# Kernel optimization log

Hardware: AMD Instinct MI355X
Metric: run time of the kernel (lower is better)

## Reference

```python
import jax, jax.numpy as jnp
import numpy as np

B, N, DIM = 4, 2048, 1024
HEADS, DHEAD = 16, 64
INNER = HEADS * DHEAD  # 1024


def _sigma(t):
    # elu(x) + 1 feature map (strictly positive)
    return jax.nn.elu(t) + 1.0


def setup_inputs() -> dict:
    key = jax.random.key(0)
    k1, k2, k3, k4, k5 = jax.random.split(key, 5)
    x = jax.random.normal(k1, (B, N, DIM), dtype=jnp.float32)
    M = jax.random.normal(k2, (B, HEADS, DHEAD, DHEAD), dtype=jnp.float32)
    Z = jnp.ones((B, HEADS, DHEAD, 1), dtype=jnp.float32)
    W_qkv = jax.random.normal(k3, (DIM, 3 * INNER), dtype=jnp.float32) * (DIM ** -0.5)
    beta_lin = jnp.ones((1,), dtype=jnp.float32) * 4.6     # Linear_Attention.beta
    beta_gate = jax.random.normal(k4, (1, HEADS, 1, 1), dtype=jnp.float32)  # per-head gate
    return {"x": x, "M": M, "Z": Z, "W_qkv": W_qkv, "beta_lin": beta_lin, "beta_gate": beta_gate}


def reference(x, M, Z, W_qkv, beta_lin, beta_gate):
    b, n, _ = x.shape
    scale = DHEAD ** -0.5

    qkv = x @ W_qkv                                   # [b, n, 3*inner]
    q, k, v = jnp.split(qkv, 3, axis=-1)
    # b n (h d) -> b h n d
    to_heads = lambda t: t.reshape(b, n, HEADS, DHEAD).transpose(0, 2, 1, 3)
    q, k, v = to_heads(q), to_heads(k), to_heads(v)

    # ---- linear-attention compressive memory branch ----
    sq = _sigma(q)                                    # [b h n d]
    sk = _sigma(k)
    A_mem = jnp.einsum('bhnd,bhdv->bhnv', sq, M) / jnp.einsum('bhnd,bhdi->bhni', sq, Z)
    moment = jnp.einsum('bhnd,bhdv->bhnv', sk, M) / jnp.einsum('bhnd,bhdi->bhni', sk, Z)

    # EMA state update (training path)
    beta_m = jnp.clip(jax.nn.sigmoid(beta_lin), 0.9, 0.999)  # scalar in (0.9, 0.999)
    Z_new = beta_m * Z + jnp.sum(sk, axis=-2)[..., None]      # [b h d 1]
    M_new = beta_m * M + jnp.einsum('bhnd,bhnv->bhdv', sk, v - moment)

    # ---- standard dot-product attention branch ----
    dots = jnp.einsum('bhid,bhjd->bhij', q, k) * scale
    attn = jax.nn.softmax(dots, axis=-1)
    A_dot = jnp.einsum('bhij,bhjd->bhid', attn, v)

    # ---- learned per-head gate ----
    g = jax.nn.sigmoid(beta_gate)                     # [1 h 1 1]
    A = g * A_mem + (1.0 - g) * A_dot                 # [b h n d]
    A = A.transpose(0, 2, 1, 3).reshape(b, n, INNER)  # b h n d -> b n (h d)
    return (A, M_new, Z_new)
```

## Files before the change

kernel.cpp:

```cpp
#include <hip/hip_runtime.h>
#include <math.h>

#define B_ 4
#define N_ 2048
#define DIM_ 1024
#define H_ 16
#define D_ 64
#define INNER_ 1024
#define BH_ (B_*H_)

#define A_ELEMS  (B_*N_*INNER_)
#define M_ELEMS  (BH_*D_*D_)
#define Z_ELEMS  (BH_*D_)

#define SC_LOG2E 0.18033688011112042f

typedef __attribute__((ext_vector_type(8))) short short8;
typedef __attribute__((ext_vector_type(4))) float f32x4;
typedef __attribute__((ext_vector_type(4))) unsigned short us4;
typedef unsigned short u16;

typedef const unsigned int __attribute__((address_space(1))) gu32;
typedef unsigned int __attribute__((address_space(3))) su32;

__device__ __forceinline__ u16 f2bf(float f) {
    unsigned int u = __float_as_uint(f);
    u += 0x7fffu + ((u >> 16) & 1u);
    return (u16)(u >> 16);
}
__device__ __forceinline__ float bf2f(u16 s) {
    return __uint_as_float(((unsigned int)s) << 16);
}
__device__ __forceinline__ float sigma_f(float x) {
    return x > 0.f ? x + 1.f : __expf(x);
}
__device__ __forceinline__ short8 sig8(short8 in) {
    short8 out;
    u16* ip = (u16*)&in; u16* op = (u16*)&out;
    #pragma unroll
    for (int c = 0; c < 8; c++) op[c] = f2bf(sigma_f(bf2f(ip[c])));
    return out;
}

__global__ __launch_bounds__(256) void cvt_x(const float* __restrict__ x,
                                             u16* __restrict__ xb) {
    long i = ((long)blockIdx.x * 256 + threadIdx.x) * 4;
    float4 f = *(const float4*)&x[i];
    us4 o = {f2bf(f.x), f2bf(f.y), f2bf(f.z), f2bf(f.w)};
    *(us4*)&xb[i] = o;
}

__global__ __launch_bounds__(256) void cvt_w(const float* __restrict__ W,
                                             u16* __restrict__ Wt) {
    __shared__ u16 T[64 * 68];
    const int t  = threadIdx.x;
    const int n0 = blockIdx.x * 64, k0 = blockIdx.y * 64;
    #pragma unroll
    for (int i = 0; i < 4; i++) {
        int r  = (t >> 4) + i * 16;
        int c4 = (t & 15) * 4;
        float4 f = *(const float4*)&W[(long)(k0 + r) * 3072 + n0 + c4];
        T[(c4 + 0) * 68 + r] = f2bf(f.x);
        T[(c4 + 1) * 68 + r] = f2bf(f.y);
        T[(c4 + 2) * 68 + r] = f2bf(f.z);
        T[(c4 + 3) * 68 + r] = f2bf(f.w);
    }
    __syncthreads();
    #pragma unroll
    for (int i = 0; i < 4; i++) {
        int n  = (t >> 4) + i * 16;
        int k4 = (t & 15) * 4;
        us4 o;
        o.x = T[n * 68 + k4];     o.y = T[n * 68 + k4 + 1];
        o.z = T[n * 68 + k4 + 2]; o.w = T[n * 68 + k4 + 3];
        *(us4*)&Wt[(long)(n0 + n) * 1024 + k0 + k4] = o;
    }
}

__global__ __launch_bounds__(256) void qkv_mfma(
    const u16* __restrict__ xb, const u16* __restrict__ Wt,
    u16* __restrict__ q, u16* __restrict__ k, u16* __restrict__ v,
    u16* __restrict__ qs) {
    __shared__ u16 As[128 * 64];
    __shared__ u16 Bs[128 * 64];
    const int t = threadIdx.x, w = t >> 6, lane = t & 63;
    const int quad = lane >> 4, l16 = lane & 15;
    const int m0 = blockIdx.y * 128, j0 = blockIdx.x * 128;
    const int mw = (w >> 1) * 64, nw = (w & 1) * 64;

    const int row0 = t >> 3;
    const int cg   = (t & 7) * 8;

    f32x4 acc[4][4] = {};

    for (int k0 = 0; k0 < DIM_; k0 += 64) {
        __syncthreads();
        #pragma unroll
        for (int i = 0; i < 4; i++) {
            int r = row0 + i * 32;
            __builtin_amdgcn_global_load_lds(
                (gu32*)&xb[(long)(m0 + r) * 1024 + k0 + cg],
                (su32*)&As[r * 64 + cg], 16, 0, 0);
            __builtin_amdgcn_global_load_lds(
                (gu32*)&Wt[(long)(j0 + r) * 1024 + k0 + cg],
                (su32*)&Bs[r * 64 + cg], 16, 0, 0);
        }
        __syncthreads();

        #pragma unroll
        for (int kk = 0; kk < 2; kk++) {
            short8 af[4], bf[4];
            #pragma unroll
            for (int mt = 0; mt < 4; mt++)
                af[mt] = *(const short8*)&As[(mw + mt * 16 + l16) * 64 + kk * 32 + quad * 8];
            #pragma unroll
            for (int nt = 0; nt < 4; nt++)
                bf[nt] = *(const short8*)&Bs[(nw + nt * 16 + l16) * 64 + kk * 32 + quad * 8];
            #pragma unroll
            for (int mt = 0; mt < 4; mt++)
                #pragma unroll
                for (int nt = 0; nt < 4; nt++)
                    acc[mt][nt] = __builtin_amdgcn_mfma_f32_16x16x32_bf16(
                        af[mt], bf[nt], acc[mt][nt], 0, 0, 0);
        }
    }

    #pragma unroll
    for (int mt = 0; mt < 4; mt++) {
        #pragma unroll
        for (int r = 0; r < 4; r++) {
            int mm = m0 + mw + mt * 16 + quad * 4 + r;
            int b  = mm >> 11, n = mm & 2047;
            #pragma unroll
            for (int nt = 0; nt < 4; nt++) {
                int col   = j0 + nw + nt * 16 + l16;
                int which = col >> 10;
                int rem   = col & 1023;
                int h = rem >> 6, d = rem & 63;
                long idx = (((long)(b * H_ + h)) * N_ + n) * D_ + d;
                float a = acc[mt][nt][r];
                u16 val = f2bf(a);
                if (which == 0) {
                    q[idx]  = val;
                    qs[idx] = f2bf(a * SC_LOG2E);
                } else {
                    u16* dst = (which == 1) ? k : v;
                    dst[idx] = val;
                }
            }
        }
    }
}

__global__ __launch_bounds__(256) void vt_transpose(
    const u16* __restrict__ vb, u16* __restrict__ vT) {
    __shared__ u16 T[64 * 72];
    const int bh = blockIdx.y;
    const int n0 = blockIdx.x * 64;
    const int t  = threadIdx.x;
    const int jj = t >> 3, kg = (t & 7) * 8;
    #pragma unroll
    for (int i = 0; i < 2; i++) {
        int j = jj + i * 32;
        short8 vv = *(const short8*)&vb[(((long)bh * N_ + n0 + j) << 6) + kg];
        u16* vp = (u16*)&vv;
        int jc = j ^ kg;
        #pragma unroll
        for (int c = 0; c < 8; c++) T[(kg + c) * 72 + jc] = vp[c];
    }
    __syncthreads();
    const int d = t >> 2, sg = (t & 3) * 16, xr = d & 56;
    short8 a0 = *(const short8*)&T[d * 72 + (sg ^ xr)];
    short8 a1 = *(const short8*)&T[d * 72 + ((sg + 8) ^ xr)];
    u16* dst = vT + ((long)bh * 64 + d) * 2048 + n0 + sg;
    *(short8*)dst       = a0;
    *(short8*)(dst + 8) = a1;
}

__global__ __launch_bounds__(256) void init_mz(
    const float* __restrict__ M, const float* __restrict__ Z,
    const float* __restrict__ beta_lin,
    float* __restrict__ outM, float* __restrict__ outZ) {
    float beta = 1.f / (1.f + __expf(-beta_lin[0]));
    beta = fminf(fmaxf(beta, 0.9f), 0.999f);
    int i = blockIdx.x * 256 + threadIdx.x;
    if (i < M_ELEMS) outM[i] = beta * M[i];
    if (i < Z_ELEMS) outZ[i] = beta * Z[i];
}

__global__ __launch_bounds__(256) void linear_mfma(
    const u16* __restrict__ qg, const u16* __restrict__ kg_,
    const u16* __restrict__ vTg, const float* __restrict__ Mg,
    const float* __restrict__ Zg, const float* __restrict__ beta_gate,
    float* __restrict__ outA, float* __restrict__ outM, float* __restrict__ outZ) {
    __shared__ u16 MTz[80 * 72];
    __shared__ u16 sqsh[64 * 72];
    __shared__ u16 sksh[64 * 72];
    __shared__ u16 skT[64 * 72];
    __shared__ u16 vT[64 * 72];
    __shared__ u16 vmT[80 * 72];
    __shared__ float dks[64];

    const int bh = blockIdx.y, b = bh >> 4, h = bh & 15;
    const int t = threadIdx.x, w = t >> 6, lane = t & 63;
    const int quad = lane >> 4, l16 = lane & 15;
    const long bhN = (long)bh * N_;

    #pragma unroll
    for (int i = 0; i < 4; i++) {
        int d  = (t >> 4) + i * 16;
        int c4 = (t & 15) * 4;
        float4 f = *(const float4*)&Mg[bh * 4096 + d * 64 + c4];
        MTz[(c4 + 0) * 72 + d] = f2bf(f.x);
        MTz[(c4 + 1) * 72 + d] = f2bf(f.y);
        MTz[(c4 + 2) * 72 + d] = f2bf(f.z);
        MTz[(c4 + 3) * 72 + d] = f2bf(f.w);
    }
    if (t < 64) {
        MTz[64 * 72 + t] = f2bf(Zg[bh * 64 + t]);
        vmT[64 * 72 + t] = f2bf(1.0f);
    }
    for (int e = t; e < 15 * 72; e += 256) {
        MTz[65 * 72 + e] = 0;
        vmT[65 * 72 + e] = 0;
    }
    if (t >= 64 && t < 72) { MTz[64 * 72 + t] = 0; vmT[64 * 72 + t] = 0; }

    const float g = 1.f / (1.f + __expf(-beta_gate[h]));

    f32x4 macc[5] = {};

    const int jj = t >> 3;
    const int kgp = (t & 7) * 8;
    const int srow = t >> 2;
    const int sg   = (t & 3) * 16;

    for (int c0 = 0; c0 < 256; c0 += 64) {
        const int n0c = blockIdx.x * 256 + c0;
        __syncthreads();

        #pragma unroll
        for (int i = 0; i < 2; i++) {
            int j = jj + i * 32;
            long gb = ((bhN + n0c + j) << 6) + kgp;
            short8 q8 = sig8(*(const short8*)&qg[gb]);
            short8 k8 = sig8(*(const short8*)&kg_[gb]);
            *(short8*)&sqsh[j * 72 + kgp] = q8;
            *(short8*)&sksh[j * 72 + kgp] = k8;
            u16* kp = (u16*)&k8;
            int jc = j ^ kgp;
            #pragma unroll
            for (int c = 0; c < 8; c++) skT[(kgp + c) * 72 + jc] = kp[c];
        }
        {
            const u16* vp = vTg + ((long)bh * 64 + srow) * 2048 + n0c + sg;
            *(short8*)&vT[srow * 72 + sg]     = *(const short8*)vp;
            *(short8*)&vT[srow * 72 + sg + 8] = *(const short8*)(vp + 8);
        }
        __syncthreads();

        {
            short8 a0 = *(const short8*)&sqsh[(w * 16 + l16) * 72 + quad * 8];
            short8 a1 = *(const short8*)&sqsh[(w * 16 + l16) * 72 + 32 + quad * 8];
            f32x4 am[5];
            #pragma unroll
            for (int ct = 0; ct < 5; ct++) {
                short8 b0 = *(const short8*)&MTz[(ct * 16 + l16) * 72 + quad * 8];
                short8 b1 = *(const short8*)&MTz[(ct * 16 + l16) * 72 + 32 + quad * 8];
                f32x4 acc = {};
                acc = __builtin_amdgcn_mfma_f32_16x16x32_bf16(a0, b0, acc, 0, 0, 0);
                acc = __builtin_amdgcn_mfma_f32_16x16x32_bf16(a1, b1, acc, 0, 0, 0);
                am[ct] = acc;
            }
            #pragma unroll
            for (int r = 0; r < 4; r++) {
                float dq  = __shfl(am[4][r], lane & 48, 64);
                float inv = __builtin_amdgcn_rcpf(dq);
                int n = n0c + w * 16 + quad * 4 + r;
                long row = ((long)(b * N_ + n)) * INNER_ + h * 64;
                #pragma unroll
                for (int ct = 0; ct < 4; ct++)
                    outA[row + ct * 16 + l16] = g * am[ct][r] * inv;
            }
        }

        f32x4 mt_[4];
        {
            short8 a0 = *(const short8*)&MTz[(w * 16 + l16) * 72 + quad * 8];
            short8 a1 = *(const short8*)&MTz[(w * 16 + l16) * 72 + 32 + quad * 8];
            #pragma unroll
            for (int ct = 0; ct < 4; ct++) {
                short8 b0 = *(const short8*)&sksh[(ct * 16 + l16) * 72 + quad * 8];
                short8 b1 = *(const short8*)&sksh[(ct * 16 + l16) * 72 + 32 + quad * 8];
                f32x4 acc = {};
                acc = __builtin_amdgcn_mfma_f32_16x16x32_bf16(a0, b0, acc, 0, 0, 0);
                acc = __builtin_amdgcn_mfma_f32_16x16x32_bf16(a1, b1, acc, 0, 0, 0);
                mt_[ct] = acc;
            }
            short8 z0 = *(const short8*)&MTz[(64 + l16) * 72 + quad * 8];
            short8 z1 = *(const short8*)&MTz[(64 + l16) * 72 + 32 + quad * 8];
            short8 b0 = *(const short8*)&sksh[(w * 16 + l16) * 72 + quad * 8];
            short8 b1 = *(const short8*)&sksh[(w * 16 + l16) * 72 + 32 + quad * 8];
            f32x4 acc = {};
            acc = __builtin_amdgcn_mfma_f32_16x16x32_bf16(z0, b0, acc, 0, 0, 0);
            acc = __builtin_amdgcn_mfma_f32_16x16x32_bf16(z1, b1, acc, 0, 0, 0);
            if (quad == 0) dks[w * 16 + l16] = __builtin_amdgcn_rcpf(acc[0]);
        }
        __syncthreads();

        #pragma unroll
        for (int ct = 0; ct < 4; ct++) {
            float invdk = dks[ct * 16 + l16];
            #pragma unroll
            for (int r = 0; r < 4; r++) {
                int vd = w * 16 + quad * 4 + r;
                float vv = bf2f(vT[vd * 72 + ct * 16 + l16]);
                vmT[vd * 72 + ct * 16 + l16] = f2bf(vv - mt_[ct][r] * invdk);
            }
        }
        __syncthreads();

        {
            int drow = w * 16 + l16, xr = drow & 56;
            short8 a0 = *(const short8*)&skT[drow * 72 + ((quad * 8) ^ xr)];
            short8 a1 = *(const short8*)&skT[drow * 72 + ((32 + quad * 8) ^ xr)];
            #pragma unroll
            for (int ct = 0; ct < 5; ct++) {
                short8 b0 = *(const short8*)&vmT[(ct * 16 + l16) * 72 + quad * 8];
                short8 b1 = *(const short8*)&vmT[(ct * 16 + l16) * 72 + 32 + quad * 8];
                macc[ct] = __builtin_amdgcn_mfma_f32_16x16x32_bf16(a0, b0, macc[ct], 0, 0, 0);
                macc[ct] = __builtin_amdgcn_mfma_f32_16x16x32_bf16(a1, b1, macc[ct], 0, 0, 0);
            }
        }
    }

    #pragma unroll
    for (int ct = 0; ct < 4; ct++)
        #pragma unroll
        for (int r = 0; r < 4; r++) {
            int d = w * 16 + quad * 4 + r;
            atomicAdd(&outM[bh * 4096 + d * 64 + ct * 16 + l16], macc[ct][r]);
        }
    if (l16 == 0)
        #pragma unroll
        for (int r = 0; r < 4; r++)
            atomicAdd(&outZ[bh * 64 + w * 16 + quad * 4 + r], macc[4][r]);
}

__global__ __launch_bounds__(256) void flash_mfma(
    const u16* __restrict__ qsb, const u16* __restrict__ kb,
    const u16* __restrict__ vTg, const float* __restrict__ beta_gate,
    float* __restrict__ outA) {
    __shared__ u16 Ks[64 * 72];
    __shared__ u16 Vt[64 * 72];

    const int bh = blockIdx.y, b = bh >> 4, h = bh & 15;
    const int n0 = blockIdx.x * 128;
    const int t = threadIdx.x, w = t >> 6, lane = t & 63;
    const int quad = lane >> 4, l16 = lane & 15;
    const long bhN = (long)bh * N_;

    const int srow = t >> 2;
    const int sg   = (t & 3) * 16;
    const int jloc = srow & 31;
    const int krow = (srow & 32) + ((jloc & 4) << 2) + ((jloc >> 3) << 2) + (jloc & 3);

    const u16* kbase  = kb + (bhN << 6);
    const u16* vtbase = vTg + (long)bh * 64 * 2048;

    short8 qf[2][2];
    #pragma unroll
    for (int mi = 0; mi < 2; mi++) {
        long qrow = bhN + n0 + w * 32 + mi * 16 + l16;
        qf[mi][0] = *(const short8*)&qsb[(qrow << 6) + quad * 8];
        qf[mi][1] = *(const short8*)&qsb[(qrow << 6) + 32 + quad * 8];
    }

    const short8 onesf = {0x3F80, 0x3F80, 0x3F80, 0x3F80,
                          0x3F80, 0x3F80, 0x3F80, 0x3F80};

    short8 kr0, kr1, vr0, vr1;
    {
        const u16* kp = kbase + ((long)srow << 6) + sg;
        kr0 = *(const short8*)kp;
        kr1 = *(const short8*)(kp + 8);
        const u16* vp = vtbase + (long)srow * 2048 + sg;
        vr0 = *(const short8*)vp;
        vr1 = *(const short8*)(vp + 8);
    }

    f32x4 of[2][4] = {};
    f32x4 ol[2] = {};

    for (int j0 = 0; j0 < N_; j0 += 64) {
        __syncthreads();
        *(short8*)&Ks[krow * 72 + sg]     = kr0;
        *(short8*)&Ks[krow * 72 + sg + 8] = kr1;
        *(short8*)&Vt[srow * 72 + sg]     = vr0;
        *(short8*)&Vt[srow * 72 + sg + 8] = vr1;
        __syncthreads();

        if (j0 + 64 < N_) {
            const u16* kp = kbase + ((long)(j0 + 64 + srow) << 6) + sg;
            kr0 = *(const short8*)kp;
            kr1 = *(const short8*)(kp + 8);
            const u16* vp = vtbase + (long)srow * 2048 + j0 + 64 + sg;
            vr0 = *(const short8*)vp;
            vr1 = *(const short8*)(vp + 8);
        }

        #pragma unroll
        for (int g = 0; g < 2; g++) {
            const int rb = g * 32;
            short8 kA0 = *(const short8*)&Ks[(rb + l16) * 72 + quad * 8];
            short8 kA1 = *(const short8*)&Ks[(rb + l16) * 72 + 32 + quad * 8];
            short8 kB0 = *(const short8*)&Ks[(rb + 16 + l16) * 72 + quad * 8];
            short8 kB1 = *(const short8*)&Ks[(rb + 16 + l16) * 72 + 32 + quad * 8];
            short8 vf[4];
            #pragma unroll
            for (int nt = 0; nt < 4; nt++)
                vf[nt] = *(const short8*)&Vt[(nt * 16 + l16) * 72 + rb + quad * 8];

            #pragma unroll
            for (int mi = 0; mi < 2; mi++) {
                f32x4 st0 = {}, st1 = {};
                st0 = __builtin_amdgcn_mfma_f32_16x16x32_bf16(kA0, qf[mi][0], st0, 0, 0, 0);
                st0 = __builtin_amdgcn_mfma_f32_16x16x32_bf16(kA1, qf[mi][1], st0, 0, 0, 0);
                st1 = __builtin_amdgcn_mfma_f32_16x16x32_bf16(kB0, qf[mi][0], st1, 0, 0, 0);
                st1 = __builtin_amdgcn_mfma_f32_16x16x32_bf16(kB1, qf[mi][1], st1, 0, 0, 0);
                float p0 = __builtin_amdgcn_exp2f(st0[0]);
                float p1 = __builtin_amdgcn_exp2f(st0[1]);
                float p2 = __builtin_amdgcn_exp2f(st0[2]);
                float p3 = __builtin_amdgcn_exp2f(st0[3]);
                float p4 = __builtin_amdgcn_exp2f(st1[0]);
                float p5 = __builtin_amdgcn_exp2f(st1[1]);
                float p6 = __builtin_amdgcn_exp2f(st1[2]);
                float p7 = __builtin_amdgcn_exp2f(st1[3]);
                short8 af;
                unsigned int* au = (unsigned int*)&af;
                au[0] = __builtin_amdgcn_perm(__float_as_uint(p1), __float_as_uint(p0),
                                              0x07060302u);
                au[1] = __builtin_amdgcn_perm(__float_as_uint(p3), __float_as_uint(p2),
                                              0x07060302u);
                au[2] = __builtin_amdgcn_perm(__float_as_uint(p5), __float_as_uint(p4),
                                              0x07060302u);
                au[3] = __builtin_amdgcn_perm(__float_as_uint(p7), __float_as_uint(p6),
                                              0x07060302u);
                ol[mi] = __builtin_amdgcn_mfma_f32_16x16x32_bf16(af, onesf, ol[mi], 0, 0, 0);
                #pragma unroll
                for (int nt = 0; nt < 4; nt++)
                    of[mi][nt] = __builtin_amdgcn_mfma_f32_16x16x32_bf16(
                        af, vf[nt], of[mi][nt], 0, 0, 0);
            }
        }
    }

    const float g  = 1.f / (1.f + __expf(-beta_gate[h]));
    const float gi = 1.f - g;
    #pragma unroll
    for (int mi = 0; mi < 2; mi++) {
        #pragma unroll
        for (int r = 0; r < 4; r++) {
            float sc = gi / ol[mi][r];
            int n = n0 + w * 32 + mi * 16 + quad * 4 + r;
            #pragma unroll
            for (int nt = 0; nt < 4; nt++) {
                long idx = ((long)(b * N_ + n)) * INNER_ + h * 64 + nt * 16 + l16;
                outA[idx] += sc * of[mi][nt][r];
            }
        }
    }
}

extern "C" void kernel_launch(void* const* d_in, const int* in_sizes, int n_in,
                              void* d_out, int out_size, void* d_ws, size_t ws_size,
                              hipStream_t stream) {
    const float* x         = (const float*)d_in[0];
    const float* M         = (const float*)d_in[1];
    const float* Z         = (const float*)d_in[2];
    const float* W         = (const float*)d_in[3];
    const float* beta_lin  = (const float*)d_in[4];
    const float* beta_gate = (const float*)d_in[5];

    float* out  = (float*)d_out;
    float* outA = out;
    float* outM = out + A_ELEMS;
    float* outZ = out + A_ELEMS + M_ELEMS;

    u16* xb = (u16*)d_ws;
    u16* Wt = xb + (size_t)8192 * 1024;
    u16* qb = Wt + (size_t)3072 * 1024;
    u16* kb = qb + (size_t)BH_ * N_ * D_;
    u16* vb = kb + (size_t)BH_ * N_ * D_;
    u16* vt = vb + (size_t)BH_ * N_ * D_;
    u16* qs = vt + (size_t)BH_ * N_ * D_;

    cvt_x<<<dim3(A_ELEMS / 1024), 256, 0, stream>>>(x, xb);
    cvt_w<<<dim3(48, 16), 256, 0, stream>>>(W, Wt);
    qkv_mfma<<<dim3(24, 64), 256, 0, stream>>>(xb, Wt, qb, kb, vb, qs);
    vt_transpose<<<dim3(N_ / 64, BH_), 256, 0, stream>>>(vb, vt);
    init_mz<<<dim3((M_ELEMS + 255) / 256), 256, 0, stream>>>(M, Z, beta_lin, outM, outZ);
    linear_mfma<<<dim3(8, BH_), 256, 0, stream>>>(qb, kb, vt, M, Z, beta_gate,
                                                  outA, outM, outZ);
    flash_mfma<<<dim3(N_ / 128, BH_), 256, 0, stream>>>(qs, kb, vt, beta_gate, outA);
}
```

Baseline: 294.2 us.

## Double-buffer QKV GEMM, swizzle block order for XCDs, drop scaled-Q buffer

The QKV GEMM now uses a double-buffered LDS pipeline with 32-wide K tiles, so the next tile's global-to-LDS load overlaps the current tile's MFMAs, with one barrier per iteration. Both the GEMM and the flash kernel switch to a 1D grid with an XCD-aware swizzle (lin&7 spread) to improve L2 locality across the MI355X chiplets. The separate pre-scaled Q buffer is removed: the scale is applied inside flash before exp2, which saves one global write stream in the GEMM epilogue but adds a multiply per score element.

```diff
diff --git a/kernel.cpp b/kernel.cpp
--- a/kernel.cpp
+++ b/kernel.cpp
@@ -79,50 +79,67 @@
 
 __global__ __launch_bounds__(256) void qkv_mfma(
     const u16* __restrict__ xb, const u16* __restrict__ Wt,
-    u16* __restrict__ q, u16* __restrict__ k, u16* __restrict__ v,
-    u16* __restrict__ qs) {
-    __shared__ u16 As[128 * 64];
-    __shared__ u16 Bs[128 * 64];
+    u16* __restrict__ q, u16* __restrict__ k, u16* __restrict__ v) {
+    __shared__ u16 As[2][128 * 32];
+    __shared__ u16 Bs[2][128 * 32];
     const int t = threadIdx.x, w = t >> 6, lane = t & 63;
     const int quad = lane >> 4, l16 = lane & 15;
-    const int m0 = blockIdx.y * 128, j0 = blockIdx.x * 128;
+
+    const int lin = blockIdx.x;
+    const int wg  = (lin & 7) * 192 + (lin >> 3);
+    const int j0  = (wg % 24) * 128;
+    const int m0  = (wg / 24) * 128;
     const int mw = (w >> 1) * 64, nw = (w & 1) * 64;
 
-    const int row0 = t >> 3;
-    const int cg   = (t & 7) * 8;
+    const int srow = t >> 2;
+    const int scol = (t & 3) * 8;
 
     f32x4 acc[4][4] = {};
 
-    for (int k0 = 0; k0 < DIM_; k0 += 64) {
-        __syncthreads();
-        #pragma unroll
-        for (int i = 0; i < 4; i++) {
-            int r = row0 + i * 32;
-            __builtin_amdgcn_global_load_lds(
-                (gu32*)&xb[(long)(m0 + r) * 1024 + k0 + cg],
-                (su32*)&As[r * 64 + cg], 16, 0, 0);
-            __builtin_amdgcn_global_load_lds(
-                (gu32*)&Wt[(long)(j0 + r) * 1024 + k0 + cg],
-                (su32*)&Bs[r * 64 + cg], 16, 0, 0);
-        }
-        __syncthreads();
-
-        #pragma unroll
-        for (int kk = 0; kk < 2; kk++) {
-            short8 af[4], bf[4];
-            #pragma unroll
-            for (int mt = 0; mt < 4; mt++)
-                af[mt] = *(const short8*)&As[(mw + mt * 16 + l16) * 64 + kk * 32 + quad * 8];
+    #pragma unroll
+    for (int i = 0; i < 2; i++) {
+        int r = srow + i * 64;
+        __builtin_amdgcn_global_load_lds(
+            (gu32*)&xb[(long)(m0 + r) * 1024 + scol],
+            (su32*)&As[0][r * 32 + scol], 16, 0, 0);
+        __builtin_amdgcn_global_load_lds(
+            (gu32*)&Wt[(long)(j0 + r) * 1024 + scol],
+            (su32*)&Bs[0][r * 32 + scol], 16, 0, 0);
+    }
+    __syncthreads();
+
+    for (int kt = 0; kt < 32; ++kt) {
+        const int cur = kt & 1;
+        if (kt + 1 < 32) {
+            const int nxt = cur ^ 1;
+            const int k0 = (kt + 1) * 32;
+            #pragma unroll
+            for (int i = 0; i < 2; i++) {
+                int r = srow + i * 64;
+                __builtin_amdgcn_global_load_lds(
+                    (gu32*)&xb[(long)(m0 + r) * 1024 + k0 + scol],
+                    (su32*)&As[nxt][r * 32 + scol], 16, 0, 0);
+                __builtin_amdgcn_global_load_lds(
+                    (gu32*)&Wt[(long)(j0 + r) * 1024 + k0 + scol],
+                    (su32*)&Bs[nxt][r * 32 + scol], 16, 0, 0);
+            }
+        }
+
+        short8 af[4], bf[4];
+        #pragma unroll
+        for (int mt = 0; mt < 4; mt++)
+            af[mt] = *(const short8*)&As[cur][(mw + mt * 16 + l16) * 32 + quad * 8];
+        #pragma unroll
+        for (int nt = 0; nt < 4; nt++)
+            bf[nt] = *(const short8*)&Bs[cur][(nw + nt * 16 + l16) * 32 + quad * 8];
+        #pragma unroll
+        for (int mt = 0; mt < 4; mt++)
             #pragma unroll
             for (int nt = 0; nt < 4; nt++)
-                bf[nt] = *(const short8*)&Bs[(nw + nt * 16 + l16) * 64 + kk * 32 + quad * 8];
-            #pragma unroll
-            for (int mt = 0; mt < 4; mt++)
-                #pragma unroll
-                for (int nt = 0; nt < 4; nt++)
-                    acc[mt][nt] = __builtin_amdgcn_mfma_f32_16x16x32_bf16(
-                        af[mt], bf[nt], acc[mt][nt], 0, 0, 0);
-        }
+                acc[mt][nt] = __builtin_amdgcn_mfma_f32_16x16x32_bf16(
+                    af[mt], bf[nt], acc[mt][nt], 0, 0, 0);
+
+        __syncthreads();
     }
 
     #pragma unroll
@@ -138,15 +155,9 @@
                 int rem   = col & 1023;
                 int h = rem >> 6, d = rem & 63;
                 long idx = (((long)(b * H_ + h)) * N_ + n) * D_ + d;
-                float a = acc[mt][nt][r];
-                u16 val = f2bf(a);
-                if (which == 0) {
-                    q[idx]  = val;
-                    qs[idx] = f2bf(a * SC_LOG2E);
-                } else {
-                    u16* dst = (which == 1) ? k : v;
-                    dst[idx] = val;
-                }
+                u16 val = f2bf(acc[mt][nt][r]);
+                u16* dst = (which == 0) ? q : (which == 1) ? k : v;
+                dst[idx] = val;
             }
         }
     }
@@ -348,14 +359,17 @@
 }
 
 __global__ __launch_bounds__(256) void flash_mfma(
-    const u16* __restrict__ qsb, const u16* __restrict__ kb,
+    const u16* __restrict__ qb, const u16* __restrict__ kb,
     const u16* __restrict__ vTg, const float* __restrict__ beta_gate,
     float* __restrict__ outA) {
     __shared__ u16 Ks[64 * 72];
     __shared__ u16 Vt[64 * 72];
 
-    const int bh = blockIdx.y, b = bh >> 4, h = bh & 15;
-    const int n0 = blockIdx.x * 128;
+    const int lin = blockIdx.x;
+    const int wg  = (lin & 7) * 128 + (lin >> 3);
+    const int bh  = wg >> 4;
+    const int n0  = (wg & 15) * 128;
+    const int b = bh >> 4, h = bh & 15;
     const int t = threadIdx.x, w = t >> 6, lane = t & 63;
     const int quad = lane >> 4, l16 = lane & 15;
     const long bhN = (long)bh * N_;
@@ -372,8 +386,8 @@
     #pragma unroll
     for (int mi = 0; mi < 2; mi++) {
         long qrow = bhN + n0 + w * 32 + mi * 16 + l16;
-        qf[mi][0] = *(const short8*)&qsb[(qrow << 6) + quad * 8];
-        qf[mi][1] = *(const short8*)&qsb[(qrow << 6) + 32 + quad * 8];
+        qf[mi][0] = *(const short8*)&qb[(qrow << 6) + quad * 8];
+        qf[mi][1] = *(const short8*)&qb[(qrow << 6) + 32 + quad * 8];
     }
 
     const short8 onesf = {0x3F80, 0x3F80, 0x3F80, 0x3F80,
@@ -428,14 +442,14 @@
                 st0 = __builtin_amdgcn_mfma_f32_16x16x32_bf16(kA1, qf[mi][1], st0, 0, 0, 0);
                 st1 = __builtin_amdgcn_mfma_f32_16x16x32_bf16(kB0, qf[mi][0], st1, 0, 0, 0);
                 st1 = __builtin_amdgcn_mfma_f32_16x16x32_bf16(kB1, qf[mi][1], st1, 0, 0, 0);
-                float p0 = __builtin_amdgcn_exp2f(st0[0]);
-                float p1 = __builtin_amdgcn_exp2f(st0[1]);
-                float p2 = __builtin_amdgcn_exp2f(st0[2]);
-                float p3 = __builtin_amdgcn_exp2f(st0[3]);
-                float p4 = __builtin_amdgcn_exp2f(st1[0]);
-                float p5 = __builtin_amdgcn_exp2f(st1[1]);
-                float p6 = __builtin_amdgcn_exp2f(st1[2]);
-                float p7 = __builtin_amdgcn_exp2f(st1[3]);
+                float p0 = __builtin_amdgcn_exp2f(st0[0] * SC_LOG2E);
+                float p1 = __builtin_amdgcn_exp2f(st0[1] * SC_LOG2E);
+                float p2 = __builtin_amdgcn_exp2f(st0[2] * SC_LOG2E);
+                float p3 = __builtin_amdgcn_exp2f(st0[3] * SC_LOG2E);
+                float p4 = __builtin_amdgcn_exp2f(st1[0] * SC_LOG2E);
+                float p5 = __builtin_amdgcn_exp2f(st1[1] * SC_LOG2E);
+                float p6 = __builtin_amdgcn_exp2f(st1[2] * SC_LOG2E);
+                float p7 = __builtin_amdgcn_exp2f(st1[3] * SC_LOG2E);
                 short8 af;
                 unsigned int* au = (unsigned int*)&af;
                 au[0] = __builtin_amdgcn_perm(__float_as_uint(p1), __float_as_uint(p0),
@@ -493,14 +507,13 @@
     u16* kb = qb + (size_t)BH_ * N_ * D_;
     u16* vb = kb + (size_t)BH_ * N_ * D_;
     u16* vt = vb + (size_t)BH_ * N_ * D_;
-    u16* qs = vt + (size_t)BH_ * N_ * D_;
 
     cvt_x<<<dim3(A_ELEMS / 1024), 256, 0, stream>>>(x, xb);
     cvt_w<<<dim3(48, 16), 256, 0, stream>>>(W, Wt);
-    qkv_mfma<<<dim3(24, 64), 256, 0, stream>>>(xb, Wt, qb, kb, vb, qs);
+    qkv_mfma<<<dim3(1536), 256, 0, stream>>>(xb, Wt, qb, kb, vb);
     vt_transpose<<<dim3(N_ / 64, BH_), 256, 0, stream>>>(vb, vt);
     init_mz<<<dim3((M_ELEMS + 255) / 256), 256, 0, stream>>>(M, Z, beta_lin, outM, outZ);
     linear_mfma<<<dim3(8, BH_), 256, 0, stream>>>(qb, kb, vt, M, Z, beta_gate,
                                                   outA, outM, outZ);
-    flash_mfma<<<dim3(N_ / 128, BH_), 256, 0, stream>>>(qs, kb, vt, beta_gate, outA);
-}
+    flash_mfma<<<dim3(N_ / 128 * BH_), 256, 0, stream>>>(qb, kb, vt, beta_gate, outA);
+}
```

Result: no change. 292.4 us (-0.6%).
